# Optimization experiments

Hardware: AMD Instinct MI355X
Metric: run time of the kernel (lower is better)

Reference implementation:

```python
import jax, jax.numpy as jnp
import numpy as np

E, K, H, I = 8, 2, 1024, 3584  # num_experts, top_k, hidden, intermediate


def setup_inputs() -> dict:
    key = jax.random.key(0)
    k0, k1, k2, k3, k4 = jax.random.split(key, 5)
    scale = 0.02
    return {
        "hidden_states": jax.random.normal(k0, (2, 1024, H), dtype=jnp.float32),
        "w_gate": jax.random.normal(k1, (E, H), dtype=jnp.float32) * scale,  # gate Linear H->E
        "w1": jax.random.normal(k2, (E, I, H), dtype=jnp.float32) * scale,   # gate proj
        "w3": jax.random.normal(k3, (E, I, H), dtype=jnp.float32) * scale,   # up proj
        "w2": jax.random.normal(k4, (E, H, I), dtype=jnp.float32) * scale,   # down proj
    }


def reference(hidden_states, w_gate, w1, w3, w2):
    B, S, Hd = hidden_states.shape
    x = hidden_states.reshape(-1, Hd)                       # [T, H]
    logits = jnp.einsum('th,eh->te', x, w_gate)             # router logits [T, E]
    probs = jax.nn.softmax(logits, axis=-1)
    topw, topi = jax.lax.top_k(probs, K)                    # [T, K]
    topw = topw / jnp.sum(topw, axis=-1, keepdims=True)     # renormalize=True
    # dense combine weights [T, E] (zero off the top-k)
    comb = jnp.sum(jax.nn.one_hot(topi, E, dtype=x.dtype) * topw[..., None], axis=1)
    # SwiGLU experts (dense reference over all experts; math matches dispatch+combine)
    g = jnp.einsum('th,eih->eti', x, w1)                    # [E, T, I]
    u = jnp.einsum('th,eih->eti', x, w3)
    h = jax.nn.silu(g) * u
    out = jnp.einsum('eti,ehi->eth', h, w2)                 # [E, T, H]
    y = jnp.einsum('te,eth->th', comb, out)                 # weighted combine
    return y.reshape(B, S, Hd)
```

## Files before the change

### kernel.cpp

```cpp
#include <hip/hip_runtime.h>
#include <hip/hip_bf16.h>
#include <stdint.h>

#define NEXP 8
#define HD 1024
#define ID 3584
#define NTOK 2048
#define NSLOT 4096
#define SLOT_PAD 128
#define NSLOT_ALLOC (NSLOT + SLOT_PAD)
#define WN (NEXP * ID * HD)
#define KSPLIT 4
#define KLEN (ID / KSPLIT)

typedef unsigned short u16;
typedef __attribute__((ext_vector_type(8))) short s16x8;
typedef __attribute__((ext_vector_type(4))) short s16x4;
typedef __attribute__((ext_vector_type(4))) float f32x4;

#define BARRIER() __builtin_amdgcn_s_barrier()
#define LGKM0()   asm volatile("s_waitcnt lgkmcnt(0)" ::: "memory")
#define VMCNT(n)  asm volatile("s_waitcnt vmcnt(" #n ")" ::: "memory")
#define SCHEDB()  __builtin_amdgcn_sched_barrier(0)

__device__ __forceinline__ u16 f2bf(float f) {
    __hip_bfloat16 h = __float2bfloat16(f);
    union { __hip_bfloat16 h; u16 u; } v; v.h = h; return v.u;
}

__device__ __forceinline__ s16x8 cvt8(f32x4 a, f32x4 b) {
    s16x8 o;
    o[0]=(short)f2bf(a[0]); o[1]=(short)f2bf(a[1]); o[2]=(short)f2bf(a[2]); o[3]=(short)f2bf(a[3]);
    o[4]=(short)f2bf(b[0]); o[5]=(short)f2bf(b[1]); o[6]=(short)f2bf(b[2]); o[7]=(short)f2bf(b[3]);
    return o;
}

__device__ __forceinline__ void glds16(const void* g, void* l) {
    __builtin_amdgcn_global_load_lds((const __attribute__((address_space(1))) unsigned*)g,
                                     (__attribute__((address_space(3))) unsigned*)l, 16, 0, 0);
}

__global__ void init_kernel(int* __restrict__ counts) {
    if (threadIdx.x < 16) counts[threadIdx.x] = 0;
}

__global__ void router_kernel(const float* __restrict__ x, const float* __restrict__ wg,
                              int* __restrict__ topk_idx, float* __restrict__ topk_w,
                              int* __restrict__ counts) {
    int t = blockIdx.x;
    int lane = threadIdx.x;
    const float* xr = x + (size_t)t * HD;
    float acc[NEXP];
#pragma unroll
    for (int e = 0; e < NEXP; ++e) acc[e] = 0.f;
#pragma unroll
    for (int i = 0; i < HD / 256; ++i) {
        int h = i * 256 + lane * 4;
        f32x4 xv = *(const f32x4*)(xr + h);
#pragma unroll
        for (int e = 0; e < NEXP; ++e) {
            f32x4 wv = *(const f32x4*)(wg + e * HD + h);
            acc[e] += xv[0]*wv[0] + xv[1]*wv[1] + xv[2]*wv[2] + xv[3]*wv[3];
        }
    }
#pragma unroll
    for (int e = 0; e < NEXP; ++e) {
#pragma unroll
        for (int s = 32; s > 0; s >>= 1) acc[e] += __shfl_xor(acc[e], s, 64);
    }
    if (lane == 0) {
        int b0 = 0; float l0 = acc[0];
#pragma unroll
        for (int e = 1; e < NEXP; ++e) if (acc[e] > l0) { l0 = acc[e]; b0 = e; }
        int b1 = (b0 == 0) ? 1 : 0; float l1 = acc[b1];
#pragma unroll
        for (int e = 0; e < NEXP; ++e) {
            if (e == b0 || e == b1) continue;
            if (acc[e] > l1) { l1 = acc[e]; b1 = e; }
        }
        float w0 = 1.f / (1.f + expf(l1 - l0));
        float w1 = 1.f - w0;
        topk_idx[2 * t] = b0; topk_idx[2 * t + 1] = b1;
        topk_w[2 * t] = w0;  topk_w[2 * t + 1] = w1;
        atomicAdd(&counts[b0], 1);
        atomicAdd(&counts[b1], 1);
    }
}

__global__ void scan_kernel(const int* __restrict__ counts, int* __restrict__ offsets,
                            int* __restrict__ rows) {
    if (threadIdx.x == 0) {
        int off = 0;
#pragma unroll
        for (int e = 0; e < NEXP; ++e) { offsets[e] = off; off += counts[e]; }
    }
    if (threadIdx.x < SLOT_PAD) rows[NSLOT + threadIdx.x] = 0;
}

__global__ void assign_kernel(const int* __restrict__ topk_idx, const int* __restrict__ offsets,
                              int* __restrict__ counts2, int* __restrict__ rows,
                              int* __restrict__ slot_of) {
    int i = blockIdx.x * 256 + threadIdx.x;
    int e = topk_idx[i];
    int pos = atomicAdd(&counts2[e], 1);
    int slot = offsets[e] + pos;
    rows[slot] = i >> 1;
    slot_of[i] = slot;
}

__global__ __launch_bounds__(256)
void cvt_bf_kernel(const float* __restrict__ src, u16* __restrict__ dst, int n8) {
    int stride = gridDim.x * 256;
    for (int i = blockIdx.x * 256 + threadIdx.x; i < n8; i += stride) {
        f32x4 v0 = ((const f32x4*)src)[2 * i];
        f32x4 v1 = ((const f32x4*)src)[2 * i + 1];
        ((s16x8*)dst)[i] = cvt8(v0, v1);
    }
}

#define G1_BLOCKS (NEXP * (NTOK / 128) * (ID / 128))
#define CVT2_BLOCKS 1024
__global__ __launch_bounds__(256, 2)
void gemm1_kernel(const u16* __restrict__ xbf, const u16* __restrict__ w1bf,
                  const u16* __restrict__ w3bf, const int* __restrict__ counts,
                  const int* __restrict__ offsets, const int* __restrict__ rows,
                  u16* __restrict__ hbuf,
                  const float* __restrict__ w2, u16* __restrict__ w2bf) {
    __shared__ u16 As[2][128][32];
    __shared__ u16 B1s[2][128][32];
    __shared__ u16 B3s[2][128][32];

    if (blockIdx.x >= G1_BLOCKS) {
        const int stride = CVT2_BLOCKS * 256;
        for (int i = (blockIdx.x - G1_BLOCKS) * 256 + threadIdx.x; i < WN / 8; i += stride) {
            f32x4 v0 = ((const f32x4*)w2)[2 * i];
            f32x4 v1 = ((const f32x4*)w2)[2 * i + 1];
            ((s16x8*)w2bf)[i] = cvt8(v0, v1);
        }
        return;
    }

    const int NT = ID / 128;
    int bid = blockIdx.x;
    int e = bid / (16 * NT);
    int rem = bid - e * (16 * NT);
    int mt = rem / NT;
    int nt = rem - mt * NT;
    int n_e = counts[e];
    int m0 = mt * 128;
    if (m0 >= n_e) return;
    int off = offsets[e];
    int n0 = nt * 128;

    int tid = threadIdx.x;
    int lane = tid & 63;
    int wid = tid >> 6;

    int srow = wid * 32 + (lane >> 2);
    int chunk = ((lane & 3) ^ ((srow >> 1) & 3)) * 8;

    int tokA0 = rows[off + m0 + srow];
    int tokA1 = rows[off + m0 + srow + 16];
    const u16* srcA0 = xbf + (size_t)tokA0 * HD + chunk;
    const u16* srcA1 = xbf + (size_t)tokA1 * HD + chunk;
    const u16* srcB1a = w1bf + ((size_t)e * ID + n0 + srow) * HD + chunk;
    const u16* srcB1b = srcB1a + (size_t)16 * HD;
    const u16* srcB3a = w3bf + ((size_t)e * ID + n0 + srow) * HD + chunk;
    const u16* srcB3b = srcB3a + (size_t)16 * HD;

    f32x4 accg[4][4] = {}, accu[4][4] = {};
    int wm = (wid >> 1) * 64, wn = (wid & 1) * 64;
    int lr = lane & 15;
    int k8sw = ((lane >> 4) ^ ((lr >> 1) & 3)) * 8;

#define STAGE1(b, k0)                                         \
    do {                                                      \
        glds16(srcA0 + (k0),  &As[b][wid * 32][0]);           \
        glds16(srcA1 + (k0),  &As[b][wid * 32 + 16][0]);      \
        glds16(srcB1a + (k0), &B1s[b][wid * 32][0]);          \
        glds16(srcB1b + (k0), &B1s[b][wid * 32 + 16][0]);     \
        glds16(srcB3a + (k0), &B3s[b][wid * 32][0]);          \
        glds16(srcB3b + (k0), &B3s[b][wid * 32 + 16][0]);     \
    } while (0)

    STAGE1(0, 0);
    STAGE1(1, 32);
    VMCNT(6);
    BARRIER();

    const int NIT = HD / 32;
#pragma unroll 2
    for (int it = 0; it < NIT; ++it) {
        int cur = it & 1;
        s16x8 a[4], b1[4], b3[4];
#pragma unroll
        for (int f = 0; f < 4; ++f) {
            a[f]  = *(const s16x8*)&As[cur][wm + f * 16 + lr][k8sw];
            b1[f] = *(const s16x8*)&B1s[cur][wn + f * 16 + lr][k8sw];
            b3[f] = *(const s16x8*)&B3s[cur][wn + f * 16 + lr][k8sw];
        }
#pragma unroll
        for (int fm = 0; fm < 4; ++fm)
#pragma unroll
            for (int fn = 0; fn < 4; ++fn) {
                accg[fm][fn] = __builtin_amdgcn_mfma_f32_16x16x32_bf16(a[fm], b1[fn], accg[fm][fn], 0, 0, 0);
                accu[fm][fn] = __builtin_amdgcn_mfma_f32_16x16x32_bf16(a[fm], b3[fn], accu[fm][fn], 0, 0, 0);
            }
        if (it + 1 < NIT) {
            LGKM0();
            BARRIER();
            SCHEDB();
            if (it + 2 < NIT) {
                STAGE1(cur, (it + 2) * 32);
                VMCNT(6);
            } else {
                VMCNT(0);
            }
            BARRIER();
        }
    }

    int lc = lane & 15;
    int lr4 = (lane >> 4) * 4;
#pragma unroll
    for (int fm = 0; fm < 4; ++fm) {
#pragma unroll
        for (int r = 0; r < 4; ++r) {
            int row = wm + fm * 16 + lr4 + r;
            if (m0 + row < n_e) {
                size_t base = (size_t)(off + m0 + row) * ID + n0 + wn;
#pragma unroll
                for (int fn = 0; fn < 4; ++fn) {
                    float g = accg[fm][fn][r];
                    float u = accu[fm][fn][r];
                    float hv = g * u / (1.f + expf(-g));
                    hbuf[base + fn * 16 + lc] = f2bf(hv);
                }
            }
        }
    }
}

__global__ __launch_bounds__(256, 2)
void gemm2_kernel(const u16* __restrict__ hbuf, const u16* __restrict__ w2bf,
                  const int* __restrict__ counts, const int* __restrict__ offsets,
                  float* __restrict__ out2) {
    const int NT = HD / 128;
    int bid = blockIdx.x;
    int e = bid / (16 * NT * KSPLIT);
    int rem = bid - e * (16 * NT * KSPLIT);
    int mt = rem / (NT * KSPLIT);
    int rem2 = rem - mt * (NT * KSPLIT);
    int nt = rem2 / KSPLIT;
    int ks = rem2 - nt * KSPLIT;
    int n_e = counts[e];
    int m0 = mt * 128;
    if (m0 >= n_e) return;
    int off = offsets[e];
    int n0 = nt * 128;
    int kbase = ks * KLEN;

    __shared__ u16 As[2][128][32];
    __shared__ u16 Bs[2][128][32];

    int tid = threadIdx.x;
    int lane = tid & 63;
    int wid = tid >> 6;

    int srow = wid * 32 + (lane >> 2);
    int chunk = ((lane & 3) ^ ((srow >> 1) & 3)) * 8;
    const u16* srcA0 = hbuf + (size_t)(off + m0 + srow) * ID + kbase + chunk;
    const u16* srcA1 = srcA0 + (size_t)16 * ID;
    const u16* srcB0 = w2bf + ((size_t)e * HD + n0 + srow) * ID + kbase + chunk;
    const u16* srcB1 = srcB0 + (size_t)16 * ID;

    f32x4 acc[4][4] = {};
    int wm = (wid >> 1) * 64, wn = (wid & 1) * 64;
    int lr = lane & 15;
    int k8sw = ((lane >> 4) ^ ((lr >> 1) & 3)) * 8;

#define STAGE2(b, k0)                                       \
    do {                                                    \
        glds16(srcA0 + (k0), &As[b][wid * 32][0]);          \
        glds16(srcA1 + (k0), &As[b][wid * 32 + 16][0]);     \
        glds16(srcB0 + (k0), &Bs[b][wid * 32][0]);          \
        glds16(srcB1 + (k0), &Bs[b][wid * 32 + 16][0]);     \
    } while (0)

    STAGE2(0, 0);
    STAGE2(1, 32);
    VMCNT(4);
    BARRIER();

    const int NIT = KLEN / 32;
#pragma unroll 2
    for (int it = 0; it < NIT; ++it) {
        int cur = it & 1;
        s16x8 a[4], b[4];
#pragma unroll
        for (int f = 0; f < 4; ++f) {
            a[f] = *(const s16x8*)&As[cur][wm + f * 16 + lr][k8sw];
            b[f] = *(const s16x8*)&Bs[cur][wn + f * 16 + lr][k8sw];
        }
#pragma unroll
        for (int fm = 0; fm < 4; ++fm)
#pragma unroll
            for (int fn = 0; fn < 4; ++fn)
                acc[fm][fn] = __builtin_amdgcn_mfma_f32_16x16x32_bf16(a[fm], b[fn], acc[fm][fn], 0, 0, 0);
        if (it + 1 < NIT) {
            LGKM0();
            BARRIER();
            SCHEDB();
            if (it + 2 < NIT) {
                STAGE2(cur, (it + 2) * 32);
                VMCNT(4);
            } else {
                VMCNT(0);
            }
            BARRIER();
        }
    }

    float* outp = out2 + (size_t)ks * NSLOT_ALLOC * HD;
    int lc = lane & 15;
    int lr4 = (lane >> 4) * 4;
#pragma unroll
    for (int fm = 0; fm < 4; ++fm) {
#pragma unroll
        for (int r = 0; r < 4; ++r) {
            int row = wm + fm * 16 + lr4 + r;
            if (m0 + row < n_e) {
                float* dst = outp + (size_t)(off + m0 + row) * HD + n0 + wn;
#pragma unroll
                for (int fn = 0; fn < 4; ++fn)
                    dst[fn * 16 + lc] = acc[fm][fn][r];
            }
        }
    }
}

__global__ void combine_kernel(const float* __restrict__ out2, const int* __restrict__ slot_of,
                               const float* __restrict__ topk_w, float* __restrict__ y) {
    int i = blockIdx.x * 256 + threadIdx.x;
    int t = i >> 8;
    int c = i & 255;
    int s0 = slot_of[2 * t], s1 = slot_of[2 * t + 1];
    float w0 = topk_w[2 * t], w1 = topk_w[2 * t + 1];
    f32x4 o = {0.f, 0.f, 0.f, 0.f};
#pragma unroll
    for (int ks = 0; ks < KSPLIT; ++ks) {
        const float* p = out2 + (size_t)ks * NSLOT_ALLOC * HD;
        f32x4 a = ((const f32x4*)(p + (size_t)s0 * HD))[c];
        f32x4 b = ((const f32x4*)(p + (size_t)s1 * HD))[c];
#pragma unroll
        for (int j = 0; j < 4; ++j) o[j] += w0 * a[j] + w1 * b[j];
    }
    ((f32x4*)(y + (size_t)t * HD))[c] = o;
}

extern "C" void kernel_launch(void* const* d_in, const int* in_sizes, int n_in,
                              void* d_out, int out_size, void* d_ws, size_t ws_size,
                              hipStream_t stream) {
    (void)in_sizes; (void)n_in; (void)out_size; (void)ws_size;
    const float* x  = (const float*)d_in[0];
    const float* wg = (const float*)d_in[1];
    const float* w1 = (const float*)d_in[2];
    const float* w3 = (const float*)d_in[3];
    const float* w2 = (const float*)d_in[4];
    float* y = (float*)d_out;

    char* ws = (char*)d_ws;
    int*   counts   = (int*)(ws + 0);
    int*   counts2  = (int*)(ws + 32);
    int*   offsets  = (int*)(ws + 64);
    int*   topk_idx = (int*)(ws + 128);
    float* topk_w   = (float*)(ws + 128 + (size_t)NSLOT * 4);
    int*   rows     = (int*)(ws + 128 + (size_t)NSLOT * 8);
    int*   slot_of  = (int*)(ws + 128 + (size_t)NSLOT * 8 + (size_t)NSLOT_ALLOC * 4);
    size_t off_xbf = 128 + (size_t)NSLOT * 12 + (size_t)NSLOT_ALLOC * 4;
    off_xbf = (off_xbf + 255) & ~(size_t)255;
    u16* xbf = (u16*)(ws + off_xbf);
    size_t off_h = off_xbf + (size_t)NTOK * HD * 2;
    u16* hbuf = (u16*)(ws + off_h);
    size_t off_w1 = off_h + (size_t)NSLOT_ALLOC * ID * 2;
    u16* w1bf = (u16*)(ws + off_w1);
    size_t off_w3 = off_w1 + (size_t)WN * 2;
    u16* w3bf = (u16*)(ws + off_w3);
    size_t off_w2 = off_w3 + (size_t)WN * 2;
    u16* w2bf = (u16*)(ws + off_w2);
    size_t off_o2 = off_w2 + (size_t)WN * 2;
    float* out2 = (float*)(ws + off_o2);

    init_kernel<<<1, 64, 0, stream>>>(counts);
    router_kernel<<<NTOK, 64, 0, stream>>>(x, wg, topk_idx, topk_w, counts);
    scan_kernel<<<1, 128, 0, stream>>>(counts, offsets, rows);
    assign_kernel<<<NSLOT / 256, 256, 0, stream>>>(topk_idx, offsets, counts2, rows, slot_of);
    cvt_bf_kernel<<<2048, 256, 0, stream>>>(x, xbf, NTOK * HD / 8);
    cvt_bf_kernel<<<2048, 256, 0, stream>>>(w1, w1bf, WN / 8);
    cvt_bf_kernel<<<2048, 256, 0, stream>>>(w3, w3bf, WN / 8);
    gemm1_kernel<<<G1_BLOCKS + CVT2_BLOCKS, 256, 0, stream>>>(xbf, w1bf, w3bf, counts, offsets, rows, hbuf, w2, w2bf);
    gemm2_kernel<<<NEXP * (NTOK / 128) * (HD / 128) * KSPLIT, 256, 0, stream>>>(hbuf, w2bf, counts, offsets, out2);
    combine_kernel<<<(NTOK * HD / 4) / 256, 256, 0, stream>>>(out2, slot_of, topk_w, y);
}
```

Before: 347.0 us.

## Fuse fp32-to-bf16 weight conversion into GEMM tile loads, drop separate convert passes

The separate passes that converted w1, w3 and w2 to bf16 are removed. The GEMMs now load fp32 weight tiles straight into registers, convert them, and write them to a single LDS buffer; only the activation tile stays double-buffered through direct global-to-LDS loads. This avoids writing and rereading about 350 MB of bf16 weight copies. In exchange each tile is converted once per M-tile instead of once overall, B reads double in bytes, and the pipelining is shallower. Gemm2's K split also drops from 4 to 2.

New measurement: 402.2 us. 15.9% more time.

```diff
diff --git a/kernel.cpp b/kernel.cpp
--- a/kernel.cpp
+++ b/kernel.cpp
@@ -9,8 +9,7 @@
 #define NSLOT 4096
 #define SLOT_PAD 128
 #define NSLOT_ALLOC (NSLOT + SLOT_PAD)
-#define WN (NEXP * ID * HD)
-#define KSPLIT 4
+#define KSPLIT 2
 #define KLEN (ID / KSPLIT)
 
 typedef unsigned short u16;
@@ -20,7 +19,7 @@
 
 #define BARRIER() __builtin_amdgcn_s_barrier()
 #define LGKM0()   asm volatile("s_waitcnt lgkmcnt(0)" ::: "memory")
-#define VMCNT(n)  asm volatile("s_waitcnt vmcnt(" #n ")" ::: "memory")
+#define VMCNT0()  asm volatile("s_waitcnt vmcnt(0)" ::: "memory")
 #define SCHEDB()  __builtin_amdgcn_sched_barrier(0)
 
 __device__ __forceinline__ u16 f2bf(float f) {
@@ -119,26 +118,14 @@
 }
 
 #define G1_BLOCKS (NEXP * (NTOK / 128) * (ID / 128))
-#define CVT2_BLOCKS 1024
 __global__ __launch_bounds__(256, 2)
-void gemm1_kernel(const u16* __restrict__ xbf, const u16* __restrict__ w1bf,
-                  const u16* __restrict__ w3bf, const int* __restrict__ counts,
+void gemm1_kernel(const u16* __restrict__ xbf, const float* __restrict__ w1,
+                  const float* __restrict__ w3, const int* __restrict__ counts,
                   const int* __restrict__ offsets, const int* __restrict__ rows,
-                  u16* __restrict__ hbuf,
-                  const float* __restrict__ w2, u16* __restrict__ w2bf) {
+                  u16* __restrict__ hbuf) {
     __shared__ u16 As[2][128][32];
-    __shared__ u16 B1s[2][128][32];
-    __shared__ u16 B3s[2][128][32];
-
-    if (blockIdx.x >= G1_BLOCKS) {
-        const int stride = CVT2_BLOCKS * 256;
-        for (int i = (blockIdx.x - G1_BLOCKS) * 256 + threadIdx.x; i < WN / 8; i += stride) {
-            f32x4 v0 = ((const f32x4*)w2)[2 * i];
-            f32x4 v1 = ((const f32x4*)w2)[2 * i + 1];
-            ((s16x8*)w2bf)[i] = cvt8(v0, v1);
-        }
-        return;
-    }
+    __shared__ u16 B1s[128][32];
+    __shared__ u16 B3s[128][32];
 
     const int NT = ID / 128;
     int bid = blockIdx.x;
@@ -158,46 +145,65 @@
 
     int srow = wid * 32 + (lane >> 2);
     int chunk = ((lane & 3) ^ ((srow >> 1) & 3)) * 8;
-
     int tokA0 = rows[off + m0 + srow];
     int tokA1 = rows[off + m0 + srow + 16];
     const u16* srcA0 = xbf + (size_t)tokA0 * HD + chunk;
     const u16* srcA1 = xbf + (size_t)tokA1 * HD + chunk;
-    const u16* srcB1a = w1bf + ((size_t)e * ID + n0 + srow) * HD + chunk;
-    const u16* srcB1b = srcB1a + (size_t)16 * HD;
-    const u16* srcB3a = w3bf + ((size_t)e * ID + n0 + srow) * HD + chunk;
-    const u16* srcB3b = srcB3a + (size_t)16 * HD;
+
+    int brow = tid >> 1;
+    int kh   = (tid & 1) * 16;
+    int bs0  = (tid & 1) * 2;
+    int swzb = (brow >> 1) & 3;
+    int g0 = (bs0 ^ swzb) * 8, g1 = ((bs0 + 1) ^ swzb) * 8;
+    const float* pB1 = w1 + ((size_t)e * ID + n0 + brow) * HD + kh;
+    const float* pB3 = w3 + ((size_t)e * ID + n0 + brow) * HD + kh;
 
     f32x4 accg[4][4] = {}, accu[4][4] = {};
     int wm = (wid >> 1) * 64, wn = (wid & 1) * 64;
     int lr = lane & 15;
     int k8sw = ((lane >> 4) ^ ((lr >> 1) & 3)) * 8;
 
-#define STAGE1(b, k0)                                         \
-    do {                                                      \
-        glds16(srcA0 + (k0),  &As[b][wid * 32][0]);           \
-        glds16(srcA1 + (k0),  &As[b][wid * 32 + 16][0]);      \
-        glds16(srcB1a + (k0), &B1s[b][wid * 32][0]);          \
-        glds16(srcB1b + (k0), &B1s[b][wid * 32 + 16][0]);     \
-        glds16(srcB3a + (k0), &B3s[b][wid * 32][0]);          \
-        glds16(srcB3b + (k0), &B3s[b][wid * 32 + 16][0]);     \
+    f32x4 rb1[4], rb3[4];
+#define LOADB(kn)                                                            \
+    do {                                                                     \
+        const float* p1 = pB1 + (kn); const float* p3 = pB3 + (kn);         \
+        rb1[0] = *(const f32x4*)(p1);      rb1[1] = *(const f32x4*)(p1+4);  \
+        rb1[2] = *(const f32x4*)(p1+8);    rb1[3] = *(const f32x4*)(p1+12); \
+        rb3[0] = *(const f32x4*)(p3);      rb3[1] = *(const f32x4*)(p3+4);  \
+        rb3[2] = *(const f32x4*)(p3+8);    rb3[3] = *(const f32x4*)(p3+12); \
     } while (0)
-
-    STAGE1(0, 0);
-    STAGE1(1, 32);
-    VMCNT(6);
+#define WRITEB()                                          \
+    do {                                                  \
+        *(s16x8*)&B1s[brow][g0] = cvt8(rb1[0], rb1[1]);   \
+        *(s16x8*)&B1s[brow][g1] = cvt8(rb1[2], rb1[3]);   \
+        *(s16x8*)&B3s[brow][g0] = cvt8(rb3[0], rb3[1]);   \
+        *(s16x8*)&B3s[brow][g1] = cvt8(rb3[2], rb3[3]);   \
+    } while (0)
+
+    glds16(srcA0, &As[0][wid * 32][0]);
+    glds16(srcA1, &As[0][wid * 32 + 16][0]);
+    LOADB(0);
+    VMCNT0();
+    WRITEB();
+    LGKM0();
     BARRIER();
 
     const int NIT = HD / 32;
 #pragma unroll 2
     for (int it = 0; it < NIT; ++it) {
         int cur = it & 1;
+        if (it + 1 < NIT) {
+            int kn = (it + 1) * 32;
+            glds16(srcA0 + kn, &As[cur ^ 1][wid * 32][0]);
+            glds16(srcA1 + kn, &As[cur ^ 1][wid * 32 + 16][0]);
+            LOADB(kn);
+        }
         s16x8 a[4], b1[4], b3[4];
 #pragma unroll
         for (int f = 0; f < 4; ++f) {
             a[f]  = *(const s16x8*)&As[cur][wm + f * 16 + lr][k8sw];
-            b1[f] = *(const s16x8*)&B1s[cur][wn + f * 16 + lr][k8sw];
-            b3[f] = *(const s16x8*)&B3s[cur][wn + f * 16 + lr][k8sw];
+            b1[f] = *(const s16x8*)&B1s[wn + f * 16 + lr][k8sw];
+            b3[f] = *(const s16x8*)&B3s[wn + f * 16 + lr][k8sw];
         }
 #pragma unroll
         for (int fm = 0; fm < 4; ++fm)
@@ -206,18 +212,15 @@
                 accg[fm][fn] = __builtin_amdgcn_mfma_f32_16x16x32_bf16(a[fm], b1[fn], accg[fm][fn], 0, 0, 0);
                 accu[fm][fn] = __builtin_amdgcn_mfma_f32_16x16x32_bf16(a[fm], b3[fn], accu[fm][fn], 0, 0, 0);
             }
+        SCHEDB();
+        BARRIER();
         if (it + 1 < NIT) {
+            VMCNT0();
+            WRITEB();
             LGKM0();
-            BARRIER();
-            SCHEDB();
-            if (it + 2 < NIT) {
-                STAGE1(cur, (it + 2) * 32);
-                VMCNT(6);
-            } else {
-                VMCNT(0);
-            }
-            BARRIER();
-        }
+        }
+        BARRIER();
+        SCHEDB();
     }
 
     int lc = lane & 15;
@@ -242,9 +245,12 @@
 }
 
 __global__ __launch_bounds__(256, 2)
-void gemm2_kernel(const u16* __restrict__ hbuf, const u16* __restrict__ w2bf,
+void gemm2_kernel(const u16* __restrict__ hbuf, const float* __restrict__ w2,
                   const int* __restrict__ counts, const int* __restrict__ offsets,
                   float* __restrict__ out2) {
+    __shared__ u16 As[2][128][32];
+    __shared__ u16 Bs[128][32];
+
     const int NT = HD / 128;
     int bid = blockIdx.x;
     int e = bid / (16 * NT * KSPLIT);
@@ -260,9 +266,6 @@
     int n0 = nt * 128;
     int kbase = ks * KLEN;
 
-    __shared__ u16 As[2][128][32];
-    __shared__ u16 Bs[2][128][32];
-
     int tid = threadIdx.x;
     int lane = tid & 63;
     int wid = tid >> 6;
@@ -271,54 +274,70 @@
     int chunk = ((lane & 3) ^ ((srow >> 1) & 3)) * 8;
     const u16* srcA0 = hbuf + (size_t)(off + m0 + srow) * ID + kbase + chunk;
     const u16* srcA1 = srcA0 + (size_t)16 * ID;
-    const u16* srcB0 = w2bf + ((size_t)e * HD + n0 + srow) * ID + kbase + chunk;
-    const u16* srcB1 = srcB0 + (size_t)16 * ID;
+
+    int brow = tid >> 1;
+    int kh   = (tid & 1) * 16;
+    int bs0  = (tid & 1) * 2;
+    int swzb = (brow >> 1) & 3;
+    int g0 = (bs0 ^ swzb) * 8, g1 = ((bs0 + 1) ^ swzb) * 8;
+    const float* pB = w2 + ((size_t)e * HD + n0 + brow) * ID + kbase + kh;
 
     f32x4 acc[4][4] = {};
     int wm = (wid >> 1) * 64, wn = (wid & 1) * 64;
     int lr = lane & 15;
     int k8sw = ((lane >> 4) ^ ((lr >> 1) & 3)) * 8;
 
-#define STAGE2(b, k0)                                       \
-    do {                                                    \
-        glds16(srcA0 + (k0), &As[b][wid * 32][0]);          \
-        glds16(srcA1 + (k0), &As[b][wid * 32 + 16][0]);     \
-        glds16(srcB0 + (k0), &Bs[b][wid * 32][0]);          \
-        glds16(srcB1 + (k0), &Bs[b][wid * 32 + 16][0]);     \
+    f32x4 rb[4];
+#define LOADB2(kn)                                                       \
+    do {                                                                 \
+        const float* p = pB + (kn);                                      \
+        rb[0] = *(const f32x4*)(p);      rb[1] = *(const f32x4*)(p+4);  \
+        rb[2] = *(const f32x4*)(p+8);    rb[3] = *(const f32x4*)(p+12); \
     } while (0)
-
-    STAGE2(0, 0);
-    STAGE2(1, 32);
-    VMCNT(4);
+#define WRITEB2()                                      \
+    do {                                               \
+        *(s16x8*)&Bs[brow][g0] = cvt8(rb[0], rb[1]);   \
+        *(s16x8*)&Bs[brow][g1] = cvt8(rb[2], rb[3]);   \
+    } while (0)
+
+    glds16(srcA0, &As[0][wid * 32][0]);
+    glds16(srcA1, &As[0][wid * 32 + 16][0]);
+    LOADB2(0);
+    VMCNT0();
+    WRITEB2();
+    LGKM0();
     BARRIER();
 
     const int NIT = KLEN / 32;
 #pragma unroll 2
     for (int it = 0; it < NIT; ++it) {
         int cur = it & 1;
+        if (it + 1 < NIT) {
+            int kn = (it + 1) * 32;
+            glds16(srcA0 + kn, &As[cur ^ 1][wid * 32][0]);
+            glds16(srcA1 + kn, &As[cur ^ 1][wid * 32 + 16][0]);
+            LOADB2(kn);
+        }
         s16x8 a[4], b[4];
 #pragma unroll
         for (int f = 0; f < 4; ++f) {
             a[f] = *(const s16x8*)&As[cur][wm + f * 16 + lr][k8sw];
-            b[f] = *(const s16x8*)&Bs[cur][wn + f * 16 + lr][k8sw];
+            b[f] = *(const s16x8*)&Bs[wn + f * 16 + lr][k8sw];
         }
 #pragma unroll
         for (int fm = 0; fm < 4; ++fm)
 #pragma unroll
             for (int fn = 0; fn < 4; ++fn)
                 acc[fm][fn] = __builtin_amdgcn_mfma_f32_16x16x32_bf16(a[fm], b[fn], acc[fm][fn], 0, 0, 0);
+        SCHEDB();
+        BARRIER();
         if (it + 1 < NIT) {
+            VMCNT0();
+            WRITEB2();
             LGKM0();
-            BARRIER();
-            SCHEDB();
-            if (it + 2 < NIT) {
-                STAGE2(cur, (it + 2) * 32);
-                VMCNT(4);
-            } else {
-                VMCNT(0);
-            }
-            BARRIER();
-        }
+        }
+        BARRIER();
+        SCHEDB();
     }
 
     float* outp = out2 + (size_t)ks * NSLOT_ALLOC * HD;
@@ -382,23 +401,16 @@
     u16* xbf = (u16*)(ws + off_xbf);
     size_t off_h = off_xbf + (size_t)NTOK * HD * 2;
     u16* hbuf = (u16*)(ws + off_h);
-    size_t off_w1 = off_h + (size_t)NSLOT_ALLOC * ID * 2;
-    u16* w1bf = (u16*)(ws + off_w1);
-    size_t off_w3 = off_w1 + (size_t)WN * 2;
-    u16* w3bf = (u16*)(ws + off_w3);
-    size_t off_w2 = off_w3 + (size_t)WN * 2;
-    u16* w2bf = (u16*)(ws + off_w2);
-    size_t off_o2 = off_w2 + (size_t)WN * 2;
+    size_t off_o2 = off_h + (size_t)NSLOT_ALLOC * ID * 2;
+    off_o2 = (off_o2 + 255) & ~(size_t)255;
     float* out2 = (float*)(ws + off_o2);
 
     init_kernel<<<1, 64, 0, stream>>>(counts);
     router_kernel<<<NTOK, 64, 0, stream>>>(x, wg, topk_idx, topk_w, counts);
     scan_kernel<<<1, 128, 0, stream>>>(counts, offsets, rows);
     assign_kernel<<<NSLOT / 256, 256, 0, stream>>>(topk_idx, offsets, counts2, rows, slot_of);
-    cvt_bf_kernel<<<2048, 256, 0, stream>>>(x, xbf, NTOK * HD / 8);
-    cvt_bf_kernel<<<2048, 256, 0, stream>>>(w1, w1bf, WN / 8);
-    cvt_bf_kernel<<<2048, 256, 0, stream>>>(w3, w3bf, WN / 8);
-    gemm1_kernel<<<G1_BLOCKS + CVT2_BLOCKS, 256, 0, stream>>>(xbf, w1bf, w3bf, counts, offsets, rows, hbuf, w2, w2bf);
-    gemm2_kernel<<<NEXP * (NTOK / 128) * (HD / 128) * KSPLIT, 256, 0, stream>>>(hbuf, w2bf, counts, offsets, out2);
+    cvt_bf_kernel<<<512, 256, 0, stream>>>(x, xbf, NTOK * HD / 8);
+    gemm1_kernel<<<G1_BLOCKS, 256, 0, stream>>>(xbf, w1, w3, counts, offsets, rows, hbuf);
+    gemm2_kernel<<<NEXP * (NTOK / 128) * (HD / 128) * KSPLIT, 256, 0, stream>>>(hbuf, w2, counts, offsets, out2);
     combine_kernel<<<(NTOK * HD / 4) / 256, 256, 0, stream>>>(out2, slot_of, topk_w, y);
 }
```
